# Performance work log

Hardware: AMD Instinct MI355X
Metric: run time of the kernel (lower is better)

The kernel has to match this reference:

```python
import jax, jax.numpy as jnp
import numpy as np

# dims: B batch, T timesteps, V nodes, D in-features, C channels, d pos-emb dim,
# TS = t_size (spatio-temporal window), P prediction steps, L layers (=4, fixed by GLU(C*4))
B, T, V, D, C, d, TS, P, L = 4, 12, 512, 1, 64, 8, 3, 12, 4
BETA = TS - 1


def setup_inputs() -> dict:
    key = jax.random.key(0)
    ks = jax.random.split(key, 30)
    n = lambda i, shape, s=1.0: jax.random.normal(ks[i], shape, dtype=jnp.float32) * s
    return dict(
        x=n(0, (B, T, V, D)),
        sape=n(1, (V, d)),
        tape=n(2, (B, T, 1, d)),
        srpe=n(3, (V, V, d)),
        trpe=n(4, (TS, 1, d)),
        zeros_x=jnp.zeros((B, BETA, V, C), jnp.float32),
        zeros_tape=jnp.zeros((B, BETA, 1, d), jnp.float32),
        range_mask=(jax.random.uniform(ks[5], (B, V, TS * V)) < 0.5).astype(jnp.float32),
        Wi=n(6, (D, C), D ** -0.5), bi=n(7, (C,), 0.02),
        gc_mu=n(8, (L, 6, d)), gc_sig=n(9, (L, 6, d), 0.5),
        Wg=n(10, (L, C, 2 * C), C ** -0.5), bg=n(11, (L, 2 * C), 0.02),
        Wsp=n(12, (L, d, 2 * C), d ** -0.5), Wtp=n(13, (L, d, 2 * C), d ** -0.5),
        fs_w=n(14, (L, C, C, T), (C * T) ** -0.5), fs_b=n(15, (L, C), 0.02),
        glu1_w=n(16, (L, 2 * C, C), C ** -0.5), glu1_b=n(17, (L, 2 * C), 0.02),
        gout_w=n(18, (8 * C, 4 * C), (4 * C) ** -0.5), gout_b=n(19, (8 * C,), 0.02),
        out_w=n(20, (P, 4 * C), (4 * C) ** -0.5), out_b=n(21, (P,), 0.02),
    )


def _glu_cv(w, b, y):
    # 1x1-conv GLU over channel dim of y: (B, Cin, V) -> (B, Cin, V)
    z = jnp.einsum('oc,bcv->bov', w, y) + b[None, :, None]
    zl, zr = jnp.split(z, 2, axis=1)
    return zl * jax.nn.sigmoid(zr)


def _forward(x, sape, tape, srpe, trpe, Wi, bi, gc_mu, gc_sig, Wg, bg, Wsp, Wtp,
             fs_w, fs_b, glu1_w, glu1_b, gout_w, gout_b, out_w, out_b,
             zeros_x, zeros_tape, range_mask):
    b_, t_ = x.shape[0], x.shape[1]
    v_ = sape.shape[0]
    ts = trpe.shape[0]
    widx = jnp.arange(t_)[:, None] + jnp.arange(ts)  # (T, t_size) sliding-window indices
    h = x @ Wi + bi                                   # InputLayer: B,T,V,C
    tape_pad = jnp.concatenate([zeros_tape, tape], axis=1)  # B,T+beta,1,d
    skips = []
    for l in range(gc_mu.shape[0]):
        mu, sig = gc_mu[l], gc_sig[l]
        gc = lambda emb, i: jnp.sum(-0.5 * (emb - mu[i]) ** 2 * sig[i] ** 2, axis=-1)
        # STPRI: Gaussian position-aware relation inference
        base = gc(sape, 0)[:, None] + gc(sape, 1)[None, :] + gc(srpe, 4)        # (V_i, V_j)
        per_t = gc(tape, 2)[:, :, 0][:, :, None] \
              + gc(tape_pad, 3)[:, :, 0][:, widx] \
              + gc(trpe, 5)[:, 0]                                               # B,T,t_size
        S = jnp.exp(per_t[:, :, :, None, None] + base)                          # B,T,k,i,j (<=1, safe)
        S = S.transpose(0, 1, 4, 2, 3).reshape(b_, t_, v_, ts * v_)             # B,T,j,(k*V+i)
        S = S * range_mask[:, None]                                             # masked relations
        # STPGConv: masked graph conv over the t_size*V window + gating
        x_pad = jnp.concatenate([zeros_x, h], axis=1)                           # B,T+beta,V,C
        xw = x_pad[:, widx].reshape(b_, t_, ts * v_, -1)                        # B,T,t_size*V,C
        g = jnp.einsum('btjm,btmc->btjc', S, xw) @ Wg[l] + bg[l]                # B,T,V,2C
        g = g + sape @ Wsp[l] + tape @ Wtp[l]                                   # +SE(V,2C) +TE(B,T,1,2C)
        gl, gr = jnp.split(g, 2, axis=-1)
        h = gl * jax.nn.sigmoid(gr)                                             # B,T,V,C
        # GFS: conv over time (kernel (1,T)) + GLU -> B,C,V
        y = jnp.einsum('bcvt,oct->bov', h.transpose(0, 3, 2, 1), fs_w[l]) + fs_b[l][None, :, None]
        skips.append(_glu_cv(glu1_w[l], glu1_b[l], y))
    s = _glu_cv(gout_w, gout_b, jnp.concatenate(skips, axis=1))                  # B,4C,V
    return jnp.einsum('oc,bcv->bov', out_w, s) + out_b[None, :, None]            # B,P,V


def reference(x, sape, tape, srpe, trpe, zeros_x, zeros_tape, range_mask, Wi, bi,
              gc_mu, gc_sig, Wg, bg, Wsp, Wtp, fs_w, fs_b, glu1_w, glu1_b,
              gout_w, gout_b, out_w, out_b):
    return _forward(x, sape, tape, srpe, trpe, Wi, bi, gc_mu, gc_sig, Wg, bg, Wsp, Wtp,
                    fs_w, fs_b, glu1_w, glu1_b, gout_w, gout_b, out_w, out_b,
                    zeros_x, zeros_tape, range_mask)
```

## Files before the change

kernel.cpp:

```cpp
#include <hip/hip_runtime.h>
#include <math.h>


typedef unsigned short u16;
typedef __attribute__((ext_vector_type(8))) short short8;
typedef __attribute__((ext_vector_type(4))) float f32x4;
typedef __attribute__((ext_vector_type(8))) unsigned short u16x8;
typedef __attribute__((ext_vector_type(4))) unsigned short u16x4;

#define MFMA16(a, b, c) __builtin_amdgcn_mfma_f32_16x16x32_bf16((a), (b), (c), 0, 0, 0)

__device__ __forceinline__ float b2f(u16 u) {
  union { unsigned int i; float f; } x; x.i = ((unsigned int)u) << 16; return x.f;
}
__device__ __forceinline__ u16 f2b(float f) {
  union { float f; unsigned int i; } x; x.f = f;
  unsigned int r = x.i + 0x7FFFu + ((x.i >> 16) & 1u);
  return (u16)(r >> 16);
}
__device__ __forceinline__ void ld8f(const float* __restrict__ p, float* f) {
  f32x4 a = *(const f32x4*)p;
  f32x4 b = *(const f32x4*)(p + 4);
  #pragma unroll
  for (int i = 0; i < 4; ++i) { f[i] = a[i]; f[4 + i] = b[i]; }
}
__device__ __forceinline__ float gcf(const float* e, const float* __restrict__ mu,
                                     const float* __restrict__ sg) {
  float s = 0.f;
  #pragma unroll
  for (int i = 0; i < 8; ++i) {
    float dm = e[i] - mu[i];
    s += dm * dm * sg[i] * sg[i];
  }
  return -0.5f * s;
}
__device__ __forceinline__ float sigm(float v) { return 1.0f / (1.0f + expf(-v)); }

__global__ __launch_bounds__(256) void prep_kernel(
    const float* __restrict__ x, const float* __restrict__ sape,
    const float* __restrict__ tape, const float* __restrict__ srpe,
    const float* __restrict__ trpe, const float* __restrict__ Wi,
    const float* __restrict__ bi, const float* __restrict__ gmu,
    const float* __restrict__ gsg, const float* __restrict__ Wg,
    const float* __restrict__ bg, const float* __restrict__ Wsp,
    const float* __restrict__ Wtp, const float* __restrict__ fsw,
    const float* __restrict__ mask,
    const float* __restrict__ g1w, const float* __restrict__ gw,
    const float* __restrict__ ow,
    u16* __restrict__ hT0, u16* __restrict__ Abf,
    float* __restrict__ spb, float* __restrict__ tpb,
    u16* __restrict__ fswT, u16* __restrict__ WgT, float* __restrict__ ev,
    u16* __restrict__ g1wB, u16* __restrict__ gwB, u16* __restrict__ owB) {
  const int tid = threadIdx.x;
  int bid = blockIdx.x;

  if (bid < 768) {
    int gid = bid * 256 + tid;
    int i8 = gid & 63, c = (gid >> 6) & 63, bt = gid >> 12;
    float xv[8];
    ld8f(&x[bt * 512 + i8 * 8], xv);
    float wic = Wi[c], bic = bi[c];
    u16x8 hv;
    #pragma unroll
    for (int ii = 0; ii < 8; ++ii) hv[ii] = f2b(xv[ii] * wic + bic);
    *(u16x8*)&hT0[gid * 8] = hv;
    return;
  }
  bid -= 768;
  if (bid < 1024) {
    int gid = bid * 256 + tid;
    int i = gid & 511, j = gid >> 9;
    float fi[8], fj[8], fr[8];
    ld8f(sape + i * 8, fi);
    ld8f(sape + j * 8, fj);
    ld8f(srpe + ((size_t)i * 512 + j) * 8, fr);
    u16 eb[4];
    #pragma unroll
    for (int l = 0; l < 4; ++l) {
      const float* mub = gmu + l * 48;
      const float* sgb = gsg + l * 48;
      float s = gcf(fi, mub + 0, sgb + 0)
              + gcf(fj, mub + 8, sgb + 8)
              + gcf(fr, mub + 32, sgb + 32);
      eb[l] = f2b(expf(s));
    }
    #pragma unroll
    for (int b = 0; b < 4; ++b)
      #pragma unroll
      for (int k = 0; k < 3; ++k) {
        float mv = mask[((size_t)(b * 512 + j)) * 1536 + k * 512 + i];
        u16 m = (mv != 0.f) ? (u16)0xFFFFu : (u16)0;
        #pragma unroll
        for (int l = 0; l < 4; ++l)
          Abf[((size_t)((l * 4 + b) * 512 + j)) * 1536 + k * 512 + i] = eb[l] & m;
      }
    return;
  }
  bid -= 1024;
  if (bid < 1024) {
    int gid = bid * 256 + tid;
    int o = gid & 127, j = (gid >> 7) & 511, l = gid >> 16;
    float a = 0.f;
    #pragma unroll
    for (int dd = 0; dd < 8; ++dd)
      a += sape[j * 8 + dd] * Wsp[(l * 8 + dd) * 128 + o];
    spb[gid] = a;
    return;
  }
  bid -= 1024;
  if (bid < 96) {
    int gid = bid * 256 + tid;
    int o = gid & 127, bt = (gid >> 7) % 48, l = gid / 6144;
    float a = bg[l * 128 + o];
    #pragma unroll
    for (int dd = 0; dd < 8; ++dd)
      a += tape[bt * 8 + dd] * Wtp[(l * 8 + dd) * 128 + o];
    tpb[gid] = a;
    return;
  }
  bid -= 96;
  if (bid < 768) {
    int gid = bid * 256 + tid;
    int kidx = gid % 768, rest = gid / 768;
    int o = rest & 63, l = rest >> 6;
    int c = kidx & 63, tt = kidx >> 6;
    fswT[gid] = f2b(fsw[((l * 64 + o) * 64 + c) * 12 + tt]);
    return;
  }
  bid -= 768;
  if (bid < 128) {
    int gid = bid * 256 + tid;
    int c = gid & 63, o = (gid >> 6) & 127, l = gid >> 13;
    WgT[gid] = f2b(Wg[(l * 64 + c) * 128 + o]);
    return;
  }
  bid -= 128;
  if (bid < 3) {
    int gid = bid * 256 + tid;
    if (gid < 576) {
      int k = gid % 3, t = (gid / 3) % 12, b = (gid / 36) % 4, l = gid / 144;
      const float* mub = gmu + l * 48;
      const float* sgb = gsg + l * 48;
      float e2[8], e3[8], e5[8];
      ld8f(tape + (b * 12 + t) * 8, e2);
      int tp = t + k - 2;
      if (tp >= 0) ld8f(tape + (b * 12 + tp) * 8, e3);
      else {
        #pragma unroll
        for (int ii = 0; ii < 8; ++ii) e3[ii] = 0.f;
      }
      ld8f(trpe + k * 8, e5);
      float s = gcf(e2, mub + 16, sgb + 16)
              + gcf(e3, mub + 24, sgb + 24)
              + gcf(e5, mub + 40, sgb + 40);
      ev[gid] = expf(s);
    }
    return;
  }
  bid -= 3;
  if (bid < 128) {
    int gid = bid * 256 + tid;
    g1wB[gid] = f2b(g1w[gid]);
    return;
  }
  bid -= 128;
  if (bid < 512) {
    int gid = bid * 256 + tid;
    gwB[gid] = f2b(gw[gid]);
    return;
  }
  bid -= 512;
  {
    int gid = bid * 256 + tid;
    if (gid < 3072) owB[gid] = f2b(ow[gid]);
  }
}

__global__ __launch_bounds__(256) void agg_kernel(
    const u16* __restrict__ Abfl, const u16* __restrict__ hT,
    u16* __restrict__ G) {
  __shared__ u16 As[128][72];
  __shared__ u16 Bs[128][72];
  const int tid = threadIdx.x, wid = tid >> 6, lane = tid & 63;
  const int l16 = lane & 15, quad = lane >> 4;
  const int bid = blockIdx.x;
  const int nt = bid % 6;
  const int mt = (bid / 6) & 3;
  const int k  = (bid / 24) % 3;
  const int b  = bid / 72;
  const int wm = wid >> 1, wn = wid & 1;

  const u16* Arow0 = Abfl + ((size_t)(b * 512 + mt * 128)) * 1536 + k * 512;
  f32x4 acc[4][4] = {};

  for (int it = 0; it < 8; ++it) {
    const int i0 = it * 64;
    #pragma unroll
    for (int s = 0; s < 4; ++s) {
      int idx = s * 256 + tid;
      int r = idx >> 3, ch = (idx & 7) * 8;
      *(u16x8*)&As[r][ch] = *(const u16x8*)&Arow0[(size_t)r * 1536 + i0 + ch];
      int tp = nt * 2 + (r >> 6), c = r & 63;
      *(u16x8*)&Bs[r][ch] =
          *(const u16x8*)&hT[((size_t)((b * 12 + tp) * 64 + c)) * 512 + i0 + ch];
    }
    __syncthreads();
    #pragma unroll
    for (int ks = 0; ks < 2; ++ks) {
      short8 af[4], bf[4];
      #pragma unroll
      for (int mb = 0; mb < 4; ++mb)
        af[mb] = *(const short8*)&As[wm * 64 + mb * 16 + l16][ks * 32 + quad * 8];
      #pragma unroll
      for (int nb = 0; nb < 4; ++nb)
        bf[nb] = *(const short8*)&Bs[wn * 64 + nb * 16 + l16][ks * 32 + quad * 8];
      #pragma unroll
      for (int mb = 0; mb < 4; ++mb)
        #pragma unroll
        for (int nb = 0; nb < 4; ++nb)
          acc[mb][nb] = MFMA16(af[mb], bf[nb], acc[mb][nb]);
    }
    __syncthreads();
  }

  u16* base = &As[0][0];
  #pragma unroll
  for (int mb = 0; mb < 4; ++mb)
    #pragma unroll
    for (int nb = 0; nb < 4; ++nb) {
      int n = wn * 64 + nb * 16 + l16;
      #pragma unroll
      for (int r = 0; r < 4; ++r) {
        int m = wm * 64 + mb * 16 + quad * 4 + r;
        base[m * 128 + n] = f2b(acc[mb][nb][r]);
      }
    }
  __syncthreads();
  u16* Gp = G + ((size_t)((b * 3 + k) * 512 + mt * 128)) * 768 + nt * 128;
  #pragma unroll
  for (int s = 0; s < 8; ++s) {
    int idx = s * 256 + tid;
    int m = idx >> 4, ch = (idx & 15) * 8;
    *(u16x8*)&Gp[(size_t)m * 768 + ch] = *(const u16x8*)&base[m * 128 + ch];
  }
}

__global__ __launch_bounds__(256) void combine_kernel(
    const u16* __restrict__ G, const float* __restrict__ evl,
    const u16* __restrict__ WgTl, const float* __restrict__ spbl,
    const float* __restrict__ tpbl, const u16* __restrict__ fswTl,
    u16* __restrict__ hTout, float* __restrict__ yptl) {
  __shared__ u16 aggL[128][72];
  __shared__ u16 hL[128][72];
  const int tid = threadIdx.x, wid = tid >> 6, lane = tid & 63;
  const int l16 = lane & 15, quad = lane >> 4;
  const int bid = blockIdx.x;
  const int mt = bid & 3;
  const int bt = bid >> 2;
  const int b = bt / 12, t = bt - b * 12;

  {
    int j = tid >> 1;
    int c0 = (tid & 1) * 32;
    float accv[32];
    #pragma unroll
    for (int ii = 0; ii < 32; ++ii) accv[ii] = 0.f;
    #pragma unroll
    for (int k = 0; k < 3; ++k) {
      int tp = t + k - 2;
      if (tp < 0) continue;
      float ek = evl[bt * 3 + k];
      const u16* gp = &G[((size_t)((b * 3 + k) * 512 + mt * 128 + j)) * 768 + tp * 64 + c0];
      #pragma unroll
      for (int s = 0; s < 4; ++s) {
        u16x8 gv = *(const u16x8*)&gp[s * 8];
        #pragma unroll
        for (int ii = 0; ii < 8; ++ii) accv[s * 8 + ii] += b2f(gv[ii]) * ek;
      }
    }
    #pragma unroll
    for (int s = 0; s < 4; ++s) {
      u16x8 ov;
      #pragma unroll
      for (int ii = 0; ii < 8; ++ii) ov[ii] = f2b(accv[s * 8 + ii]);
      *(u16x8*)&aggL[j][c0 + s * 8] = ov;
    }
  }
  __syncthreads();

  f32x4 acc2[8][2] = {};
  #pragma unroll
  for (int ks = 0; ks < 2; ++ks) {
    short8 bf[2];
    #pragma unroll
    for (int nb = 0; nb < 2; ++nb)
      bf[nb] = *(const short8*)&aggL[wid * 32 + nb * 16 + l16][ks * 32 + quad * 8];
    #pragma unroll
    for (int mb = 0; mb < 8; ++mb) {
      short8 a = *(const short8*)&WgTl[(mb * 16 + l16) * 64 + ks * 32 + quad * 8];
      acc2[mb][0] = MFMA16(a, bf[0], acc2[mb][0]);
      acc2[mb][1] = MFMA16(a, bf[1], acc2[mb][1]);
    }
  }

  #pragma unroll
  for (int mb = 0; mb < 4; ++mb) {
    int ob = mb * 16 + quad * 4;
    #pragma unroll
    for (int nb = 0; nb < 2; ++nb) {
      int jl = wid * 32 + nb * 16 + l16;
      int jg = mt * 128 + jl;
      f32x4 spl = *(const f32x4*)&spbl[jg * 128 + ob];
      f32x4 spr = *(const f32x4*)&spbl[jg * 128 + 64 + ob];
      f32x4 tpl = *(const f32x4*)&tpbl[bt * 128 + ob];
      f32x4 tpr = *(const f32x4*)&tpbl[bt * 128 + 64 + ob];
      #pragma unroll
      for (int r = 0; r < 4; ++r) {
        float vl = acc2[mb][nb][r] + spl[r] + tpl[r];
        float vr = acc2[mb + 4][nb][r] + spr[r] + tpr[r];
        u16 hb = f2b(vl * sigm(vr));
        hTout[((size_t)((b * 12 + t) * 64 + ob + r)) * 512 + jg] = hb;
        hL[jl][ob + r] = hb;
      }
    }
  }
  __syncthreads();

  f32x4 accY[4][2] = {};
  #pragma unroll
  for (int ks = 0; ks < 2; ++ks) {
    short8 bfv[2];
    #pragma unroll
    for (int nb = 0; nb < 2; ++nb)
      bfv[nb] = *(const short8*)&hL[wid * 32 + nb * 16 + l16][ks * 32 + quad * 8];
    #pragma unroll
    for (int mb = 0; mb < 4; ++mb) {
      short8 a = *(const short8*)&fswTl[(mb * 16 + l16) * 768 + t * 64 + ks * 32 + quad * 8];
      accY[mb][0] = MFMA16(a, bfv[0], accY[mb][0]);
      accY[mb][1] = MFMA16(a, bfv[1], accY[mb][1]);
    }
  }
  #pragma unroll
  for (int mb = 0; mb < 4; ++mb)
    #pragma unroll
    for (int nb = 0; nb < 2; ++nb) {
      int j = mt * 128 + wid * 32 + nb * 16 + l16;
      #pragma unroll
      for (int r = 0; r < 4; ++r) {
        int o = mb * 16 + quad * 4 + r;
        yptl[((size_t)(bt * 64 + o)) * 512 + j] = accY[mb][nb][r];
      }
    }
}

__global__ __launch_bounds__(256) void reduce_kernel(
    const float* __restrict__ ypt, const float* __restrict__ fsb,
    u16* __restrict__ yB) {
  int gid = blockIdx.x * 256 + threadIdx.x;
  int j4 = gid & 127, o = (gid >> 7) & 63, b = (gid >> 13) & 3, l = gid >> 15;
  const float* base = &ypt[(size_t)l * 1572864 +
                           ((size_t)((b * 12) * 64 + o)) * 512 + j4 * 4];
  float fb = fsb[l * 64 + o];
  f32x4 s = {fb, fb, fb, fb};
  #pragma unroll
  for (int t = 0; t < 12; ++t) s += *(const f32x4*)&base[(size_t)t * 32768];
  u16x4 pk;
  #pragma unroll
  for (int ii = 0; ii < 4; ++ii) pk[ii] = f2b(s[ii]);
  *(u16x4*)&yB[((size_t)((l * 4 + b) * 64 + o)) * 512 + j4 * 4] = pk;
}

__global__ __launch_bounds__(256) void glu1cat_kernel(
    const u16* __restrict__ yB, const u16* __restrict__ g1wB,
    const float* __restrict__ g1b, u16* __restrict__ catB) {
  __shared__ u16 yL[128][72];
  const int tid = threadIdx.x, wid = tid >> 6, lane = tid & 63;
  const int l16 = lane & 15, quad = lane >> 4;
  const int l = blockIdx.x >> 4;
  const int b = (blockIdx.x >> 2) & 3;
  const int v0 = (blockIdx.x & 3) * 128;

  {
    int o = tid & 63, sv = tid >> 6;
    const u16* src = &yB[((size_t)((l * 4 + b) * 64 + o)) * 512 + v0 + sv * 32];
    u16x8 p0 = *(const u16x8*)&src[0];
    u16x8 p1 = *(const u16x8*)&src[8];
    u16x8 p2 = *(const u16x8*)&src[16];
    u16x8 p3 = *(const u16x8*)&src[24];
    #pragma unroll
    for (int ii = 0; ii < 8; ++ii) {
      yL[sv * 32 + ii][o] = p0[ii];
      yL[sv * 32 + 8 + ii][o] = p1[ii];
      yL[sv * 32 + 16 + ii][o] = p2[ii];
      yL[sv * 32 + 24 + ii][o] = p3[ii];
    }
  }
  __syncthreads();

  f32x4 acc[2][8] = {};
  #pragma unroll
  for (int ks = 0; ks < 2; ++ks) {
    short8 a0 = *(const short8*)&g1wB[l * 8192 + (wid * 16 + l16) * 64 +
                                      ks * 32 + quad * 8];
    short8 a1 = *(const short8*)&g1wB[l * 8192 + (64 + wid * 16 + l16) * 64 +
                                      ks * 32 + quad * 8];
    #pragma unroll
    for (int nb = 0; nb < 8; ++nb) {
      short8 bf = *(const short8*)&yL[nb * 16 + l16][ks * 32 + quad * 8];
      acc[0][nb] = MFMA16(a0, bf, acc[0][nb]);
      acc[1][nb] = MFMA16(a1, bf, acc[1][nb]);
    }
  }
  #pragma unroll
  for (int nb = 0; nb < 8; ++nb) {
    int v = v0 + nb * 16 + l16;
    int oc = wid * 16 + quad * 4;
    u16x4 pk;
    #pragma unroll
    for (int r = 0; r < 4; ++r) {
      float zl = acc[0][nb][r] + g1b[l * 128 + oc + r];
      float zr = acc[1][nb][r] + g1b[l * 128 + 64 + oc + r];
      pk[r] = f2b(zl * sigm(zr));
    }
    *(u16x4*)&catB[((size_t)(b * 512 + v)) * 256 + l * 64 + oc] = pk;
  }
}

__global__ __launch_bounds__(256) void gout_kernel(
    const u16* __restrict__ catB, const u16* __restrict__ gwB,
    const float* __restrict__ gb, u16* __restrict__ sB) {
  __shared__ u16 cL[64][264];
  const int tid = threadIdx.x, wid = tid >> 6, lane = tid & 63;
  const int l16 = lane & 15, quad = lane >> 4;
  const int wm = wid >> 1, wn = wid & 1;
  const int b = blockIdx.x >> 6;
  const int v0 = ((blockIdx.x >> 3) & 7) * 64;
  const int cc0 = (blockIdx.x & 7) * 32;

  {
    int v = tid >> 2, seg = (tid & 3) * 64;
    const u16* src = &catB[((size_t)(b * 512 + v0 + v)) * 256 + seg];
    #pragma unroll
    for (int s = 0; s < 8; ++s)
      *(u16x8*)&cL[v][seg + s * 8] = *(const u16x8*)&src[s * 8];
  }
  __syncthreads();

  f32x4 acc[2][2] = {};
  #pragma unroll
  for (int ks = 0; ks < 8; ++ks) {
    short8 aL = *(const short8*)&gwB[(cc0 + wm * 16 + l16) * 256 +
                                     ks * 32 + quad * 8];
    short8 aH = *(const short8*)&gwB[(256 + cc0 + wm * 16 + l16) * 256 +
                                     ks * 32 + quad * 8];
    #pragma unroll
    for (int nb = 0; nb < 2; ++nb) {
      short8 bf = *(const short8*)&cL[wn * 32 + nb * 16 + l16][ks * 32 + quad * 8];
      acc[0][nb] = MFMA16(aL, bf, acc[0][nb]);
      acc[1][nb] = MFMA16(aH, bf, acc[1][nb]);
    }
  }
  #pragma unroll
  for (int nb = 0; nb < 2; ++nb) {
    int v = v0 + wn * 32 + nb * 16 + l16;
    int cc = cc0 + wm * 16 + quad * 4;
    u16x4 pk;
    #pragma unroll
    for (int r = 0; r < 4; ++r) {
      float zl = acc[0][nb][r] + gb[cc + r];
      float zr = acc[1][nb][r] + gb[256 + cc + r];
      pk[r] = f2b(zl * sigm(zr));
    }
    *(u16x4*)&sB[((size_t)(b * 512 + v)) * 256 + cc] = pk;
  }
}

__global__ __launch_bounds__(256) void head_kernel(
    const u16* __restrict__ sB, const u16* __restrict__ owB,
    const float* __restrict__ obv, float* __restrict__ out) {
  const int tid = threadIdx.x, wid = tid >> 6, lane = tid & 63;
  const int l16 = lane & 15, quad = lane >> 4;
  const int b = blockIdx.x >> 3;
  const int v0 = (blockIdx.x & 7) * 64;

  f32x4 acc = {};
  #pragma unroll
  for (int ks = 0; ks < 8; ++ks) {
    short8 a;
    if (l16 < 12) a = *(const short8*)&owB[l16 * 256 + ks * 32 + quad * 8];
    else {
      #pragma unroll
      for (int ii = 0; ii < 8; ++ii) a[ii] = 0;
    }
    short8 bf = *(const short8*)&sB[((size_t)(b * 512 + v0 + wid * 16 + l16)) * 256 +
                                    ks * 32 + quad * 8];
    acc = MFMA16(a, bf, acc);
  }
  #pragma unroll
  for (int r = 0; r < 4; ++r) {
    int p = quad * 4 + r;
    if (p < 12)
      out[(b * 12 + p) * 512 + v0 + wid * 16 + l16] = acc[r] + obv[p];
  }
}

extern "C" void kernel_launch(void* const* d_in, const int* in_sizes, int n_in,
                              void* d_out, int out_size, void* d_ws, size_t ws_size,
                              hipStream_t stream) {
  const float* x    = (const float*)d_in[0];
  const float* sape = (const float*)d_in[1];
  const float* tape = (const float*)d_in[2];
  const float* srpe = (const float*)d_in[3];
  const float* trpe = (const float*)d_in[4];
  const float* mask = (const float*)d_in[7];
  const float* Wi   = (const float*)d_in[8];
  const float* bi   = (const float*)d_in[9];
  const float* gmu  = (const float*)d_in[10];
  const float* gsg  = (const float*)d_in[11];
  const float* Wg   = (const float*)d_in[12];
  const float* bg   = (const float*)d_in[13];
  const float* Wsp  = (const float*)d_in[14];
  const float* Wtp  = (const float*)d_in[15];
  const float* fsw  = (const float*)d_in[16];
  const float* fsb  = (const float*)d_in[17];
  const float* g1w  = (const float*)d_in[18];
  const float* g1b  = (const float*)d_in[19];
  const float* gow  = (const float*)d_in[20];
  const float* gob  = (const float*)d_in[21];
  const float* ow   = (const float*)d_in[22];
  const float* obv  = (const float*)d_in[23];

  char* w = (char*)d_ws;
  u16*   hT_a = (u16*)(w + 0);
  u16*   hT_b = (u16*)(w + 3145728);
  u16*   Abf  = (u16*)(w + 6291456);
  u16*   G    = (u16*)(w + 31457280);
  u16*   fswT = (u16*)(w + 40894464);
  u16*   WgT  = (u16*)(w + 41287680);
  u16*   g1wB = (u16*)(w + 41353216);
  u16*   gwB  = (u16*)(w + 41418752);
  u16*   owB  = (u16*)(w + 41680896);
  float* spb  = (float*)(w + 41689088);
  float* tpb  = (float*)(w + 42737664);
  float* ev   = (float*)(w + 42835968);
  float* ypt  = (float*)(w + 42852352);
  u16*   yB   = (u16*)(w + 68018176);
  u16*   catB = (u16*)(w + 70115328);
  u16*   sB   = (u16*)(w + 71163904);

  prep_kernel<<<4463, 256, 0, stream>>>(x, sape, tape, srpe, trpe, Wi, bi, gmu, gsg,
                                        Wg, bg, Wsp, Wtp, fsw, mask, g1w, gow, ow,
                                        hT_a, Abf, spb, tpb, fswT, WgT, ev,
                                        g1wB, gwB, owB);
  u16* hin = hT_a;
  u16* hout = hT_b;
  for (int l = 0; l < 4; ++l) {
    agg_kernel<<<288, 256, 0, stream>>>(Abf + (size_t)l * 3145728, hin, G);
    combine_kernel<<<192, 256, 0, stream>>>(G, ev + l * 144, WgT + l * 8192,
                                            spb + l * 65536, tpb + l * 6144,
                                            fswT + l * 49152, hout,
                                            ypt + (size_t)l * 1572864);
    u16* tmp = hin; hin = hout; hout = tmp;
  }
  reduce_kernel<<<512, 256, 0, stream>>>(ypt, fsb, yB);
  glu1cat_kernel<<<64, 256, 0, stream>>>(yB, g1wB, g1b, catB);
  gout_kernel<<<256, 256, 0, stream>>>(catB, gwB, gob, sB);
  head_kernel<<<32, 256, 0, stream>>>(sB, owB, obv, (float*)d_out);
}
```

Measured before the change: 247.6 us.

## Fuse aggregation and combine into one layer kernel with per-tile flag waits

Merges agg_kernel and combine_kernel into a single launch per layer. Blocks 192..479 compute the aggregation GEMM tiles and publish a completion flag, while blocks 0..191 spin on flags for only the tiles they need before combining. This removes a kernel boundary and lets combine work overlap with unfinished aggregation tiles. The cost is busy-wait spinning and a dependence on producer blocks being scheduled, since lower-index consumer blocks could deadlock if they occupy all slots. It also adds a memset for the flags.

```diff
diff --git a/kernel.cpp b/kernel.cpp
--- a/kernel.cpp
+++ b/kernel.cpp
@@ -100,22 +100,22 @@
   if (bid < 1024) {
     int gid = bid * 256 + tid;
     int o = gid & 127, j = (gid >> 7) & 511, l = gid >> 16;
-    float a = 0.f;
+    float s = 0.f;
     #pragma unroll
     for (int dd = 0; dd < 8; ++dd)
-      a += sape[j * 8 + dd] * Wsp[(l * 8 + dd) * 128 + o];
-    spb[gid] = a;
+      s += sape[j * 8 + dd] * Wsp[(l * 8 + dd) * 128 + o];
+    spb[gid] = s;
     return;
   }
   bid -= 1024;
   if (bid < 96) {
     int gid = bid * 256 + tid;
     int o = gid & 127, bt = (gid >> 7) % 48, l = gid / 6144;
-    float a = bg[l * 128 + o];
+    float s = bg[l * 128 + o];
     #pragma unroll
     for (int dd = 0; dd < 8; ++dd)
-      a += tape[bt * 8 + dd] * Wtp[(l * 8 + dd) * 128 + o];
-    tpb[gid] = a;
+      s += tape[bt * 8 + dd] * Wtp[(l * 8 + dd) * 128 + o];
+    tpb[gid] = s;
     return;
   }
   bid -= 96;
@@ -176,88 +176,104 @@
   }
 }
 
-__global__ __launch_bounds__(256) void agg_kernel(
-    const u16* __restrict__ Abfl, const u16* __restrict__ hT,
-    u16* __restrict__ G) {
-  __shared__ u16 As[128][72];
-  __shared__ u16 Bs[128][72];
+__global__ __launch_bounds__(256, 2) void layer_kernel(
+    const u16* __restrict__ Abfl, const u16* __restrict__ hTin,
+    const float* __restrict__ evl, const u16* __restrict__ WgTl,
+    const float* __restrict__ spbl, const float* __restrict__ tpbl,
+    const u16* __restrict__ fswTl, u16* __restrict__ G,
+    u16* __restrict__ hTout, float* __restrict__ yptl,
+    int* __restrict__ flags) {
+  __shared__ __align__(16) char smem[36864];
   const int tid = threadIdx.x, wid = tid >> 6, lane = tid & 63;
   const int l16 = lane & 15, quad = lane >> 4;
+
+  if (blockIdx.x >= 192) {
+    const int bid = blockIdx.x - 192;
+    u16 (*As)[72] = (u16 (*)[72])smem;
+    u16 (*Bs)[72] = (u16 (*)[72])(smem + 18432);
+    const int nt = bid % 6;
+    const int mt = (bid / 6) & 3;
+    const int k  = (bid / 24) % 3;
+    const int b  = bid / 72;
+    const int wm = wid >> 1, wn = wid & 1;
+
+    const u16* Arow0 = Abfl + ((size_t)(b * 512 + mt * 128)) * 1536 + k * 512;
+    f32x4 acc[4][4] = {};
+
+    for (int it = 0; it < 8; ++it) {
+      const int i0 = it * 64;
+      #pragma unroll
+      for (int s = 0; s < 4; ++s) {
+        int idx = s * 256 + tid;
+        int r = idx >> 3, ch = (idx & 7) * 8;
+        *(u16x8*)&As[r][ch] = *(const u16x8*)&Arow0[(size_t)r * 1536 + i0 + ch];
+        int tp = nt * 2 + (r >> 6), c = r & 63;
+        *(u16x8*)&Bs[r][ch] =
+            *(const u16x8*)&hTin[((size_t)((b * 12 + tp) * 64 + c)) * 512 + i0 + ch];
+      }
+      __syncthreads();
+      #pragma unroll
+      for (int ks = 0; ks < 2; ++ks) {
+        short8 af[4], bf[4];
+        #pragma unroll
+        for (int mb = 0; mb < 4; ++mb)
+          af[mb] = *(const short8*)&As[wm * 64 + mb * 16 + l16][ks * 32 + quad * 8];
+        #pragma unroll
+        for (int nb = 0; nb < 4; ++nb)
+          bf[nb] = *(const short8*)&Bs[wn * 64 + nb * 16 + l16][ks * 32 + quad * 8];
+        #pragma unroll
+        for (int mb = 0; mb < 4; ++mb)
+          #pragma unroll
+          for (int nb = 0; nb < 4; ++nb)
+            acc[mb][nb] = MFMA16(af[mb], bf[nb], acc[mb][nb]);
+      }
+      __syncthreads();
+    }
+
+    u16* base = (u16*)smem;
+    #pragma unroll
+    for (int mb = 0; mb < 4; ++mb)
+      #pragma unroll
+      for (int nb = 0; nb < 4; ++nb) {
+        int n = wn * 64 + nb * 16 + l16;
+        #pragma unroll
+        for (int r = 0; r < 4; ++r) {
+          int m = wm * 64 + mb * 16 + quad * 4 + r;
+          base[m * 128 + n] = f2b(acc[mb][nb][r]);
+        }
+      }
+    __syncthreads();
+    u16* Gp = G + ((size_t)((b * 3 + k) * 512 + mt * 128)) * 768 + nt * 128;
+    #pragma unroll
+    for (int s = 0; s < 8; ++s) {
+      int idx = s * 256 + tid;
+      int m = idx >> 4, ch = (idx & 15) * 8;
+      *(u16x8*)&Gp[(size_t)m * 768 + ch] = *(const u16x8*)&base[m * 128 + ch];
+    }
+    __threadfence();
+    __syncthreads();
+    if (tid == 0) atomicExch(&flags[bid], 1);
+    return;
+  }
+
   const int bid = blockIdx.x;
-  const int nt = bid % 6;
-  const int mt = (bid / 6) & 3;
-  const int k  = (bid / 24) % 3;
-  const int b  = bid / 72;
-  const int wm = wid >> 1, wn = wid & 1;
-
-  const u16* Arow0 = Abfl + ((size_t)(b * 512 + mt * 128)) * 1536 + k * 512;
-  f32x4 acc[4][4] = {};
-
-  for (int it = 0; it < 8; ++it) {
-    const int i0 = it * 64;
-    #pragma unroll
-    for (int s = 0; s < 4; ++s) {
-      int idx = s * 256 + tid;
-      int r = idx >> 3, ch = (idx & 7) * 8;
-      *(u16x8*)&As[r][ch] = *(const u16x8*)&Arow0[(size_t)r * 1536 + i0 + ch];
-      int tp = nt * 2 + (r >> 6), c = r & 63;
-      *(u16x8*)&Bs[r][ch] =
-          *(const u16x8*)&hT[((size_t)((b * 12 + tp) * 64 + c)) * 512 + i0 + ch];
-    }
-    __syncthreads();
-    #pragma unroll
-    for (int ks = 0; ks < 2; ++ks) {
-      short8 af[4], bf[4];
-      #pragma unroll
-      for (int mb = 0; mb < 4; ++mb)
-        af[mb] = *(const short8*)&As[wm * 64 + mb * 16 + l16][ks * 32 + quad * 8];
-      #pragma unroll
-      for (int nb = 0; nb < 4; ++nb)
-        bf[nb] = *(const short8*)&Bs[wn * 64 + nb * 16 + l16][ks * 32 + quad * 8];
-      #pragma unroll
-      for (int mb = 0; mb < 4; ++mb)
-        #pragma unroll
-        for (int nb = 0; nb < 4; ++nb)
-          acc[mb][nb] = MFMA16(af[mb], bf[nb], acc[mb][nb]);
-    }
-    __syncthreads();
-  }
-
-  u16* base = &As[0][0];
-  #pragma unroll
-  for (int mb = 0; mb < 4; ++mb)
-    #pragma unroll
-    for (int nb = 0; nb < 4; ++nb) {
-      int n = wn * 64 + nb * 16 + l16;
-      #pragma unroll
-      for (int r = 0; r < 4; ++r) {
-        int m = wm * 64 + mb * 16 + quad * 4 + r;
-        base[m * 128 + n] = f2b(acc[mb][nb][r]);
-      }
-    }
-  __syncthreads();
-  u16* Gp = G + ((size_t)((b * 3 + k) * 512 + mt * 128)) * 768 + nt * 128;
-  #pragma unroll
-  for (int s = 0; s < 8; ++s) {
-    int idx = s * 256 + tid;
-    int m = idx >> 4, ch = (idx & 15) * 8;
-    *(u16x8*)&Gp[(size_t)m * 768 + ch] = *(const u16x8*)&base[m * 128 + ch];
-  }
-}
-
-__global__ __launch_bounds__(256) void combine_kernel(
-    const u16* __restrict__ G, const float* __restrict__ evl,
-    const u16* __restrict__ WgTl, const float* __restrict__ spbl,
-    const float* __restrict__ tpbl, const u16* __restrict__ fswTl,
-    u16* __restrict__ hTout, float* __restrict__ yptl) {
-  __shared__ u16 aggL[128][72];
-  __shared__ u16 hL[128][72];
-  const int tid = threadIdx.x, wid = tid >> 6, lane = tid & 63;
-  const int l16 = lane & 15, quad = lane >> 4;
-  const int bid = blockIdx.x;
+  u16 (*aggL)[72] = (u16 (*)[72])smem;
+  u16 (*hL)[72]   = (u16 (*)[72])(smem + 18432);
   const int mt = bid & 3;
   const int bt = bid >> 2;
   const int b = bt / 12, t = bt - b * 12;
+
+  if (tid == 0) {
+    #pragma unroll
+    for (int k = 0; k < 3; ++k) {
+      int tp = t + k - 2;
+      if (tp < 0) continue;
+      int tile = b * 72 + k * 24 + mt * 6 + (tp >> 1);
+      while (atomicAdd(&flags[tile], 0) == 0) __builtin_amdgcn_s_sleep(4);
+    }
+    __threadfence();
+  }
+  __syncthreads();
 
   {
     int j = tid >> 1;
@@ -547,7 +563,9 @@
   u16*   yB   = (u16*)(w + 68018176);
   u16*   catB = (u16*)(w + 70115328);
   u16*   sB   = (u16*)(w + 71163904);
-
+  int*   flags= (int*)(w + 72212480);
+
+  hipMemsetAsync(flags, 0, 4 * 288 * sizeof(int), stream);
   prep_kernel<<<4463, 256, 0, stream>>>(x, sape, tape, srpe, trpe, Wi, bi, gmu, gsg,
                                         Wg, bg, Wsp, Wtp, fsw, mask, g1w, gow, ow,
                                         hT_a, Abf, spb, tpb, fswT, WgT, ev,
@@ -555,11 +573,12 @@
   u16* hin = hT_a;
   u16* hout = hT_b;
   for (int l = 0; l < 4; ++l) {
-    agg_kernel<<<288, 256, 0, stream>>>(Abf + (size_t)l * 3145728, hin, G);
-    combine_kernel<<<192, 256, 0, stream>>>(G, ev + l * 144, WgT + l * 8192,
-                                            spb + l * 65536, tpb + l * 6144,
-                                            fswT + l * 49152, hout,
-                                            ypt + (size_t)l * 1572864);
+    layer_kernel<<<480, 256, 0, stream>>>(Abf + (size_t)l * 3145728, hin,
+                                          ev + l * 144, WgT + l * 8192,
+                                          spb + l * 65536, tpb + l * 6144,
+                                          fswT + l * 49152, G, hout,
+                                          ypt + (size_t)l * 1572864,
+                                          flags + l * 288);
     u16* tmp = hin; hin = hout; hout = tmp;
   }
   reduce_kernel<<<512, 256, 0, stream>>>(ypt, fsb, yB);
```

New measurement: 401.4 us. 62.1% more time.
